# Kernel optimization log

Measured on AMD Instinct MI355X. Metric: run time of the kernel, lower is better.

## Reference

```python
import jax, jax.numpy as jnp
import numpy as np

B, L, H, NH, NE, M = 4, 1024, 768, 12, 42, 8
EMB = 768
OFFSET = 1  # bert cls offset


def setup_inputs() -> dict:
    key = jax.random.key(0)
    ks = jax.random.split(key, 6)
    seq = jax.random.normal(ks[0], (B, L, H), jnp.float32)
    attn = jax.random.uniform(ks[1], (B, NH, L, L), jnp.float32)
    attn = attn / attn.sum(-1, keepdims=True)  # row-stochastic like softmaxed attention probs
    W_head = jax.random.normal(ks[2], (2 * H, EMB), jnp.float32) * 0.02
    b_head = jnp.zeros((EMB,), jnp.float32)
    W_tail = jax.random.normal(ks[3], (2 * H, EMB), jnp.float32) * 0.02
    b_tail = jnp.zeros((EMB,), jnp.float32)
    # mention start positions (before +offset); keep start+offset < L
    mention_pos = jax.random.randint(ks[4], (B, NE, M), 0, L - OFFSET - 1)
    counts = jax.random.randint(ks[5], (B, NE), 1, M + 1)  # >=1 valid mention per entity
    mention_mask = jnp.arange(M)[None, None, :] < counts[:, :, None]
    return dict(sequence_output=seq, attention=attn, W_head=W_head, b_head=b_head,
                W_tail=W_tail, b_tail=b_tail, mention_pos=mention_pos,
                mention_mask=mention_mask)


def _get_hrt(seq, attn, mention_pos, mention_mask):
    # seq: [B,L,H]; attn: [B,NH,L,L]; mention_pos/mask: [B,NE,M]
    b_idx = jnp.arange(B)[:, None, None]
    pos = mention_pos + OFFSET                          # [B,NE,M]
    m_emb = seq[b_idx, pos]                             # [B,NE,M,H] mention embeddings
    att_t = jnp.transpose(attn, (0, 2, 1, 3))           # [B,L,NH,L]
    m_att = att_t[b_idx, pos]                           # [B,NE,M,NH,L] mention attentions
    mask = mention_mask
    neg_inf = jnp.finfo(seq.dtype).min
    # per-entity logsumexp pooling over mentions
    ent_emb = jax.nn.logsumexp(jnp.where(mask[..., None], m_emb, neg_inf), axis=2)
    has_m = mask.any(axis=2)
    ent_emb = jnp.where(has_m[..., None], ent_emb, 0.0)  # [B,NE,H]
    cnt = mask.sum(axis=2).astype(seq.dtype)
    ent_att = (m_att * mask[..., None, None].astype(seq.dtype)).sum(axis=2)
    ent_att = ent_att / jnp.maximum(cnt, 1.0)[..., None, None]  # [B,NE,NH,L] mean over mentions
    # all ordered (head, tail) pairs on the NE x NE grid
    hs = jnp.broadcast_to(ent_emb[:, :, None, :], (B, NE, NE, H))
    ts = jnp.broadcast_to(ent_emb[:, None, :, :], (B, NE, NE, H))
    # ht_att = relu(mean_h(h_att * t_att)), normalized over seq, then context = ht_att @ seq
    ht = jnp.einsum('bihl,bjhl->bijl', ent_att, ent_att) / NH  # [B,NE,NE,L]
    ht = jax.nn.relu(ht)
    ht = ht / (ht.sum(-1, keepdims=True) + 1e-10)
    rs = jnp.einsum('bijl,bld->bijd', ht, seq)                  # [B,NE,NE,H]
    return hs, rs, ts


def reference(sequence_output, attention, W_head, b_head, W_tail, b_tail, mention_pos, mention_mask):
    hs, rs, ts = _get_hrt(sequence_output, attention, mention_pos, mention_mask)
    h_out = jnp.tanh(jnp.concatenate([hs, rs], axis=-1) @ W_head + b_head)
    t_out = jnp.tanh(jnp.concatenate([ts, rs], axis=-1) @ W_tail + b_tail)
    return h_out, t_out
```

## Files before the change

### kernel.cpp

```cpp
#include <hip/hip_runtime.h>
#include <math.h>

typedef _Float16 f16;
typedef __attribute__((ext_vector_type(4))) _Float16 f16x4;
typedef __attribute__((ext_vector_type(8))) _Float16 f16x8;
typedef __attribute__((ext_vector_type(4))) float f32x4;

#define B_    4
#define L_    1024
#define H_    768
#define NH_   12
#define NE_   42
#define M_    8
#define E2_   1536
#define HTP_  1792
#define OUT_HALF 5419008LL

typedef __attribute__((address_space(1))) const unsigned char ga_t;
typedef __attribute__((address_space(3))) unsigned char la_t;
__device__ __forceinline__ void async16(const void* g, void* l) {
    __builtin_amdgcn_global_load_lds((ga_t*)g, (la_t*)l, 16, 0, 0);
}

__device__ __forceinline__ float fast_tanh(float x) {
    float e = __expf(2.f * x);
    return 1.f - 2.f / (e + 1.f);
}


__device__ void prep_body(int bid, char* smem,
                          const float* __restrict__ Wh, const float* __restrict__ Wt,
                          const float* __restrict__ bh, const float* __restrict__ bt,
                          f16* __restrict__ wtop, f16* __restrict__ wbot,
                          float* __restrict__ bcat) {
    float (*tile)[33] = (float(*)[33])smem;
    int tx = bid % 24, ty = (bid / 24) % 24, m = bid / 576;
    const float* src = (m & 1) ? Wt : Wh;
    int roff = (m & 2) ? H_ : 0;
    f16* dst = (m & 2) ? wbot : wtop;
    int coff = (m & 1) ? H_ : 0;
    int x = threadIdx.x & 31, y8 = threadIdx.x >> 5;
#pragma unroll
    for (int r = 0; r < 4; r++) {
        int h = ty*32 + y8 + r*8, c = tx*32 + x;
        tile[y8 + r*8][x] = src[(long long)(roff + h)*H_ + c];
    }
    __syncthreads();
#pragma unroll
    for (int r = 0; r < 4; r++) {
        int c2 = tx*32 + y8 + r*8, h2 = ty*32 + x;
        dst[(long long)(coff + c2)*H_ + h2] = (f16)tile[x][y8 + r*8];
    }
    if (bid == 0) {
        for (int idx = threadIdx.x; idx < E2_; idx += 256)
            bcat[idx] = (idx < H_) ? bh[idx] : bt[idx - H_];
    }
}

__device__ void seq16_body(int bid, const float* __restrict__ seq,
                           f16* __restrict__ seq16) {
    int idx = (bid*256 + threadIdx.x) * 4;
    f32x4 v = *(const f32x4*)(seq + idx);
    f16x4 o = {(f16)v[0], (f16)v[1], (f16)v[2], (f16)v[3]};
    *(f16x4*)(seq16 + idx) = o;
}

__device__ void ent_emb_body(int bid, const float* __restrict__ seq,
                             const int* __restrict__ mpos,
                             const int* __restrict__ mmask,
                             f16* __restrict__ ent) {
    int e = bid % NE_, b = bid / NE_;
    int tid = threadIdx.x;
    const int* mp = mpos  + (b*NE_ + e)*M_;
    const int* mk = mmask + (b*NE_ + e)*M_;
    int pos[M_], msk[M_];
#pragma unroll
    for (int m = 0; m < M_; m++) { msk[m] = mk[m]; pos[m] = mp[m] + 1; }
#pragma unroll
    for (int q = 0; q < 3; q++) {
        int h = tid + q*256;
        float mx = -1e30f, vals[M_];
#pragma unroll
        for (int m = 0; m < M_; m++) {
            vals[m] = 0.f;
            if (msk[m]) {
                float v = seq[((long long)b*L_ + pos[m])*H_ + h];
                vals[m] = v; mx = fmaxf(mx, v);
            }
        }
        float s = 0.f;
#pragma unroll
        for (int m = 0; m < M_; m++) if (msk[m]) s += __expf(vals[m] - mx);
        float lse = (mx > -1e29f) ? mx + __logf(s) : 0.f;
        ent[(b*NE_ + e)*H_ + h] = (f16)lse;
    }
}

__device__ void ent_att_body(int bid, const float* __restrict__ attn,
                             const int* __restrict__ mpos,
                             const int* __restrict__ mmask,
                             f16* __restrict__ eatt) {
    int nh = bid % NH_, e = (bid / NH_) % NE_, b = bid / (NH_*NE_);
    int tid = threadIdx.x;
    int l0 = tid * 4;
    const int* mp = mpos  + (b*NE_ + e)*M_;
    const int* mk = mmask + (b*NE_ + e)*M_;
    const float* abase = attn + (long long)(b*NH_ + nh) * L_ * L_;
    f32x4 acc = {0,0,0,0}; int cnt = 0;
#pragma unroll
    for (int m = 0; m < M_; m++) {
        if (mk[m]) {
            cnt++;
            const float* row = abase + (long long)(mp[m] + 1) * L_;
            acc += *(const f32x4*)(row + l0);
        }
    }
    float inv = 1.f / (float)(cnt > 0 ? cnt : 1);
    f16x4 o = {(f16)(acc[0]*inv), (f16)(acc[1]*inv), (f16)(acc[2]*inv), (f16)(acc[3]*inv)};
    *(f16x4*)(eatt + ((long long)(b*NE_ + e)*NH_ + nh)*L_ + l0) = o;
}

__device__ void ht_body(int bid, char* smem, const f16* __restrict__ eatt,
                        f16* __restrict__ HT) {
    int jg = bid % 6, i = (bid / 6) % NE_, b = bid / 252;
    int tid = threadIdx.x;
    f16* ei_s = (f16*)smem;
    float (*red)[4] = (float(*)[4])(smem + NH_*L_*2);
    const f16* ei = eatt + (long long)(b*NE_ + i)*NH_*L_;
#pragma unroll
    for (int q = 0; q < 6; q++) {
        int off = (q*256 + tid)*8;
        *(f16x8*)(ei_s + off) = *(const f16x8*)(ei + off);
    }
    __syncthreads();
    int l0 = tid*4;
    int wave = tid >> 6, lane = tid & 63;
    for (int jj = 0; jj < 7; jj++) {
        int j = jg*7 + jj;
        const f16* ej = eatt + (long long)(b*NE_ + j)*NH_*L_;
        f32x4 acc = {0,0,0,0};
#pragma unroll
        for (int h = 0; h < NH_; h++) {
            f16x4 vi = *(const f16x4*)(ei_s + h*L_ + l0);
            f16x4 vj = *(const f16x4*)(ej   + h*L_ + l0);
#pragma unroll
            for (int r = 0; r < 4; r++) acc[r] += (float)vi[r] * (float)vj[r];
        }
        float v[4]; float s = 0.f;
#pragma unroll
        for (int r = 0; r < 4; r++) {
            float t = acc[r] * (1.f/12.f);
            t = t > 0.f ? t : 0.f;
            v[r] = t; s += t;
        }
#pragma unroll
        for (int m = 1; m < 64; m <<= 1) s += __shfl_xor(s, m, 64);
        if (lane == 0) red[jj][wave] = s;
        __syncthreads();
        float S = red[jj][0] + red[jj][1] + red[jj][2] + red[jj][3];
        float sc = 1.f / (S + 1e-10f);
        f16x4 o = {(f16)(v[0]*sc), (f16)(v[1]*sc), (f16)(v[2]*sc), (f16)(v[3]*sc)};
        *(f16x4*)(HT + ((long long)b*HTP_ + i*NE_ + j)*L_ + l0) = o;
    }
}

#define LDSS 40
__device__ void gemm_het_body(int bx, int by, char* smem,
                              const f16* __restrict__ A, const f16* __restrict__ BT,
                              float* __restrict__ het, const float* __restrict__ bcat) {
    const int M = 168, K = 768;
    f16* As = (f16*)smem;
    f16* Bs = (f16*)(smem + 64*LDSS*2);
    int bm = bx*64, bn = by*64;
    int tid = threadIdx.x;
    int wave = tid >> 6, lane = tid & 63;
    int wm = (wave >> 1)*32, wn = (wave & 1)*32;
    int lo4 = lane & 15, kq = (lane >> 4)*8;
    int srow = tid >> 2, scol = (tid & 3)*8;
    bool aval = (bm + srow) < M;
    const f16* aptr = A + (long long)(bm + srow)*K + scol;
    const f16* bptr = BT + (long long)(bn + srow)*K + scol;
    f32x4 acc[2][2] = {};
    for (int k0 = 0; k0 < K; k0 += 32) {
        uint4 zero = {0,0,0,0};
        uint4 av = aval ? *(const uint4*)(aptr + k0) : zero;
        uint4 bv = *(const uint4*)(bptr + k0);
        __syncthreads();
        *(uint4*)(As + srow*LDSS + scol) = av;
        *(uint4*)(Bs + srow*LDSS + scol) = bv;
        __syncthreads();
        f16x8 a0 = *(const f16x8*)(As + (wm +      lo4)*LDSS + kq);
        f16x8 a1 = *(const f16x8*)(As + (wm + 16 + lo4)*LDSS + kq);
        f16x8 b0 = *(const f16x8*)(Bs + (wn +      lo4)*LDSS + kq);
        f16x8 b1 = *(const f16x8*)(Bs + (wn + 16 + lo4)*LDSS + kq);
        acc[0][0] = __builtin_amdgcn_mfma_f32_16x16x32_f16(a0, b0, acc[0][0], 0,0,0);
        acc[0][1] = __builtin_amdgcn_mfma_f32_16x16x32_f16(a0, b1, acc[0][1], 0,0,0);
        acc[1][0] = __builtin_amdgcn_mfma_f32_16x16x32_f16(a1, b0, acc[1][0], 0,0,0);
        acc[1][1] = __builtin_amdgcn_mfma_f32_16x16x32_f16(a1, b1, acc[1][1], 0,0,0);
    }
    int rloc = (lane >> 4)*4;
#pragma unroll
    for (int sm = 0; sm < 2; sm++)
#pragma unroll
    for (int sn = 0; sn < 2; sn++) {
        f32x4 a = acc[sm][sn];
        int c  = bn + wn + sn*16 + lo4;
        int rb = bm + wm + sm*16 + rloc;
#pragma unroll
        for (int r = 0; r < 4; r++)
            if (rb + r < M) het[(rb + r)*E2_ + c] = a[r] + bcat[c];
    }
}

template<int MODE>
__device__ void gemm2_body(int bx, int by, int bz, char* smem,
                           const f16* __restrict__ A, const f16* __restrict__ BT, int K,
                           long long strideA, long long strideBT,
                           const float* __restrict__ het, float* __restrict__ outp,
                           f16* __restrict__ outp16) {
    f16* As = (f16*)smem;
    f16* Bs = (f16*)(smem + 8192);
    int bm = bx*128, bn = by*128;
    const f16* Ab = A + strideA*bz;
    const f16* Bb = BT + strideBT*bz;
    int tid = threadIdx.x, wave = tid >> 6, lane = tid & 63;
    int wm = (wave >> 1)*64, wn = (wave & 1)*64;
    int lo4 = lane & 15, kq = (lane >> 4)*8;
    int lrow = lane >> 2, lcol = (lane & 3)*8;
    const f16* ag = Ab + (long long)(bm + wave*32 + lrow)*K + lcol;
    const f16* bg = Bb + (long long)(bn + wave*32 + lrow)*K + lcol;
    f16* asl = As + wave*1024;
    f16* bsl = Bs + wave*1024;
    f32x4 acc[4][4] = {};
    for (int k0 = 0; k0 < K; k0 += 32) {
        async16(ag + k0,          asl);
        async16(ag + k0 + 16*K,   asl + 512);
        async16(bg + k0,          bsl);
        async16(bg + k0 + 16*K,   bsl + 512);
        __syncthreads();
        f16x8 af[4], bf[4];
#pragma unroll
        for (int s = 0; s < 4; s++) {
            af[s] = *(const f16x8*)(As + (wm + s*16 + lo4)*32 + kq);
            bf[s] = *(const f16x8*)(Bs + (wn + s*16 + lo4)*32 + kq);
        }
#pragma unroll
        for (int sm = 0; sm < 4; sm++)
#pragma unroll
        for (int sn = 0; sn < 4; sn++)
            acc[sm][sn] = __builtin_amdgcn_mfma_f32_16x16x32_f16(af[sm], bf[sn], acc[sm][sn], 0,0,0);
        __syncthreads();
    }
    int rloc = (lane >> 4)*4;
#pragma unroll
    for (int sm = 0; sm < 4; sm++)
#pragma unroll
    for (int sn = 0; sn < 4; sn++) {
        f32x4 a = acc[sm][sn];
        int c  = bn + wn + sn*16 + lo4;
        int rb = bm + wm + sm*16 + rloc;
        if constexpr (MODE == 1) {
            f16x4 o = {(f16)a[0], (f16)a[1], (f16)a[2], (f16)a[3]};
            *(f16x4*)(outp16 + (long long)bz*E2_*L_ + (long long)c*L_ + rb) = o;
        } else {
#pragma unroll
            for (int r = 0; r < 4; r++) {
                int row = rb + r;
                if (row < NE_*NE_) {
                    int i = row / NE_;
                    int j = row - i*NE_;
                    int sel = (c < H_) ? i : j;
                    float bias = het[(bz*NE_ + sel)*E2_ + c];
                    float v = fast_tanh(a[r] + bias);
                    long long o = (c < H_)
                        ? ((long long)((bz*NE_ + i)*NE_ + j))*H_ + c
                        : OUT_HALF + ((long long)((bz*NE_ + i)*NE_ + j))*H_ + (c - H_);
                    outp[o] = v;
                }
            }
        }
    }
}

__global__ __launch_bounds__(256) void k_L1(
        const float* __restrict__ seq, const float* __restrict__ attn,
        const float* __restrict__ Wh, const float* __restrict__ bh,
        const float* __restrict__ Wt, const float* __restrict__ bt,
        const int* __restrict__ mpos, const int* __restrict__ mmask,
        f16* __restrict__ wtop, f16* __restrict__ wbot, float* __restrict__ bcat,
        f16* __restrict__ seq16, f16* __restrict__ ent, f16* __restrict__ eatt) {
    __shared__ __align__(16) char smem[4224];
    int bid = blockIdx.x;
    if (bid < 2304)       prep_body(bid, smem, Wh, Wt, bh, bt, wtop, wbot, bcat);
    else if (bid < 5376)  seq16_body(bid - 2304, seq, seq16);
    else if (bid < 5544)  ent_emb_body(bid - 5376, seq, mpos, mmask, ent);
    else                  ent_att_body(bid - 5544, attn, mpos, mmask, eatt);
}

__global__ __launch_bounds__(256) void k_L2(
        const f16* __restrict__ seq16, const f16* __restrict__ wbot,
        const f16* __restrict__ ent, const f16* __restrict__ wtop,
        const float* __restrict__ bcat, const f16* __restrict__ eatt,
        f16* __restrict__ seqWT, float* __restrict__ het, f16* __restrict__ HT) {
    __shared__ __align__(16) char smem[24704];
    int bid = blockIdx.x;
    if (bid < 384) {
        int bx = bid & 7, by = (bid >> 3) % 12, bz = bid / 96;
        gemm2_body<1>(bx, by, bz, smem, seq16, wbot, 768,
                      (long long)L_*H_, 0, nullptr, nullptr, seqWT);
    } else if (bid < 1392) {
        ht_body(bid - 384, smem, eatt, HT);
    } else {
        int r = bid - 1392;
        gemm_het_body(r % 3, r / 3, smem, ent, wtop, het, bcat);
    }
}

__global__ __launch_bounds__(256) void k_L3(
        const f16* __restrict__ HT, const f16* __restrict__ seqWT,
        const float* __restrict__ het, float* __restrict__ outp) {
    __shared__ __align__(16) char smem[16384];
    gemm2_body<2>(blockIdx.x, blockIdx.y, blockIdx.z, smem, HT, seqWT, 1024,
                  (long long)HTP_*L_, (long long)E2_*L_, het, outp, nullptr);
}

extern "C" void kernel_launch(void* const* d_in, const int* in_sizes, int n_in,
                              void* d_out, int out_size, void* d_ws, size_t ws_size,
                              hipStream_t stream) {
    const float* seq  = (const float*)d_in[0];
    const float* attn = (const float*)d_in[1];
    const float* Wh   = (const float*)d_in[2];
    const float* bh   = (const float*)d_in[3];
    const float* Wt   = (const float*)d_in[4];
    const float* bt   = (const float*)d_in[5];
    const int* mpos   = (const int*)d_in[6];
    const int* mmask  = (const int*)d_in[7];
    float* out = (float*)d_out;
    char* ws = (char*)d_ws;
    f16*   ent   = (f16*)  (ws + 0);
    f16*   wtop  = (f16*)  (ws + 258048);
    f16*   wbot  = (f16*)  (ws + 2617344);
    float* bcat  = (float*)(ws + 4976640);
    float* het   = (float*)(ws + 4982784);
    f16*   eatt  = (f16*)  (ws + 6014976);
    f16*   seq16 = (f16*)  (ws + 10143744);
    f16*   HT    = (f16*)  (ws + 16435200);
    f16*   seqWT = (f16*)  (ws + 31115264);

    k_L1<<<7560, 256, 0, stream>>>(seq, attn, Wh, bh, Wt, bt, mpos, mmask,
                                   wtop, wbot, bcat, seq16, ent, eatt);
    k_L2<<<1464, 256, 0, stream>>>(seq16, wbot, ent, wtop, bcat, eatt,
                                   seqWT, het, HT);
    k_L3<<<dim3(14, 12, B_), 256, 0, stream>>>(HT, seqWT, het, out);
}
```

Baseline: 360.4 us.

## Rewrite final GEMM as 256x256 tile, 8-wave kernel with async LDS double buffering

The final HT×seqWT GEMM with tanh epilogue becomes a dedicated kernel. It uses 256x256 tiles, 512 threads, and 128KB of LDS. Global-to-LDS async loads are double-buffered and interleaved per quadrant phase, with explicit vmcnt waits, barriers and setprio around the MFMA bursts, and the LDS layout is XOR-swizzled. The aim is to raise data reuse and overlap memory with MFMA. The cost is fewer blocks (168) on a large-CU GPU, heavy register and LDS pressure, and more fragile manual synchronisation.

New measurement: 371.4 us. 3.1% more time.

```diff
diff --git a/kernel.cpp b/kernel.cpp
--- a/kernel.cpp
+++ b/kernel.cpp
@@ -262,21 +262,140 @@
         if constexpr (MODE == 1) {
             f16x4 o = {(f16)a[0], (f16)a[1], (f16)a[2], (f16)a[3]};
             *(f16x4*)(outp16 + (long long)bz*E2_*L_ + (long long)c*L_ + rb) = o;
-        } else {
-#pragma unroll
-            for (int r = 0; r < 4; r++) {
-                int row = rb + r;
-                if (row < NE_*NE_) {
-                    int i = row / NE_;
-                    int j = row - i*NE_;
-                    int sel = (c < H_) ? i : j;
-                    float bias = het[(bz*NE_ + sel)*E2_ + c];
-                    float v = fast_tanh(a[r] + bias);
-                    long long o = (c < H_)
-                        ? ((long long)((bz*NE_ + i)*NE_ + j))*H_ + c
-                        : OUT_HALF + ((long long)((bz*NE_ + i)*NE_ + j))*H_ + (c - H_);
-                    outp[o] = v;
-                }
+        }
+    }
+}
+
+
+__device__ __forceinline__ void stage_regionA(const f16* __restrict__ Ab, int bm,
+                                              int t, int rq, char* ldsAbuf, int tid) {
+    int k0 = t * 64;
+    char* wbase = ldsAbuf + rq*16384 + (tid & ~63)*16;
+#pragma unroll
+    for (int ld = 0; ld < 2; ld++) {
+        int o    = (ld*512 + tid) * 16;
+        int lr   = o >> 7;
+        int colb = o & 127;
+        int grow = (lr & 63) + ((lr >> 6) << 7) + rq*64;
+        int scolb = colb ^ ((lr & 7) << 4);
+        const char* g = (const char*)(Ab + (long long)(bm + grow)*1024 + k0) + scolb;
+        async16(g, wbase + ld*8192);
+    }
+}
+
+__device__ __forceinline__ void stage_regionB(const f16* __restrict__ Bb, int bn,
+                                              int t, int cq, char* ldsBbuf, int tid) {
+    int k0 = t * 64;
+    char* wbase = ldsBbuf + cq*16384 + (tid & ~63)*16;
+#pragma unroll
+    for (int ld = 0; ld < 2; ld++) {
+        int o    = (ld*512 + tid) * 16;
+        int lr   = o >> 7;
+        int colb = o & 127;
+        int brow = ((lr >> 5)*2 + cq)*32 + (lr & 31);
+        int scolb = colb ^ ((lr & 7) << 4);
+        const char* g = (const char*)(Bb + (long long)(bn + brow)*1024 + k0) + scolb;
+        async16(g, wbase + ld*8192);
+    }
+}
+
+#define PHASE(RQ, CQ, STAGE_STMT, WAIT_STMT) do {                              \
+    f16x8 afr[4][2], bfr[2][2];                                                \
+    _Pragma("unroll")                                                          \
+    for (int i_ = 0; i_ < 4; i_++) {                                           \
+        char* pa_ = bA + (RQ)*16384 + (wr*64 + i_*16 + lo4)*128;               \
+        _Pragma("unroll")                                                      \
+        for (int ks_ = 0; ks_ < 2; ks_++)                                      \
+            afr[i_][ks_] = *(const f16x8*)(pa_ + ((ks_*64 + kq2) ^ sw));       \
+    }                                                                          \
+    _Pragma("unroll")                                                          \
+    for (int j_ = 0; j_ < 2; j_++) {                                           \
+        char* pb_ = bB + (CQ)*16384 + (wc*32 + j_*16 + lo4)*128;               \
+        _Pragma("unroll")                                                      \
+        for (int ks_ = 0; ks_ < 2; ks_++)                                      \
+            bfr[j_][ks_] = *(const f16x8*)(pb_ + ((ks_*64 + kq2) ^ sw));       \
+    }                                                                          \
+    STAGE_STMT;                                                                \
+    __builtin_amdgcn_s_barrier();                                              \
+    __builtin_amdgcn_sched_barrier(0);                                         \
+    asm volatile("" ::: "memory");                                             \
+    __builtin_amdgcn_s_setprio(1);                                             \
+    _Pragma("unroll")                                                          \
+    for (int i_ = 0; i_ < 4; i_++)                                             \
+    _Pragma("unroll")                                                          \
+    for (int j_ = 0; j_ < 2; j_++) {                                           \
+        acc[(RQ)*4+i_][(CQ)*2+j_] = __builtin_amdgcn_mfma_f32_16x16x32_f16(    \
+            afr[i_][0], bfr[j_][0], acc[(RQ)*4+i_][(CQ)*2+j_], 0,0,0);         \
+        acc[(RQ)*4+i_][(CQ)*2+j_] = __builtin_amdgcn_mfma_f32_16x16x32_f16(    \
+            afr[i_][1], bfr[j_][1], acc[(RQ)*4+i_][(CQ)*2+j_], 0,0,0);         \
+    }                                                                          \
+    __builtin_amdgcn_s_setprio(0);                                             \
+    WAIT_STMT;                                                                 \
+    __builtin_amdgcn_s_barrier();                                              \
+    __builtin_amdgcn_sched_barrier(0);                                         \
+    asm volatile("" ::: "memory");                                             \
+} while (0)
+
+__global__ __launch_bounds__(512, 2) void k_L3(
+        const f16* __restrict__ HT, const f16* __restrict__ seqWT,
+        const float* __restrict__ het, float* __restrict__ outp) {
+    __shared__ __align__(16) char smem[131072];
+    int bm = blockIdx.x*256, bn = blockIdx.y*256, bz = blockIdx.z;
+    const f16* Ab = HT + (long long)HTP_*L_*bz;
+    const f16* Bb = seqWT + (long long)E2_*L_*bz;
+    int tid = threadIdx.x, wave = tid >> 6, lane = tid & 63;
+    int wr = wave >> 2, wc = wave & 3;
+    int lo4 = lane & 15, kq2 = (lane >> 4)*16;
+    int sw = (lo4 & 7) << 4;
+    f32x4 acc[8][4] = {};
+
+    stage_regionA(Ab, bm, 0, 0, smem + 0,     tid);
+    stage_regionB(Bb, bn, 0, 0, smem + 65536, tid);
+    stage_regionB(Bb, bn, 0, 1, smem + 65536, tid);
+    stage_regionA(Ab, bm, 0, 1, smem + 0,     tid);
+    stage_regionA(Ab, bm, 1, 0, smem + 32768, tid);
+    asm volatile("s_waitcnt vmcnt(2)" ::: "memory");
+    __builtin_amdgcn_s_barrier();
+    __builtin_amdgcn_sched_barrier(0);
+    asm volatile("" ::: "memory");
+
+    for (int t = 0; t < 16; t++) {
+        char* bA  = smem + (t & 1)*32768;
+        char* bB  = smem + 65536 + (t & 1)*32768;
+        char* bA1 = smem + ((t+1) & 1)*32768;
+        char* bB1 = smem + 65536 + ((t+1) & 1)*32768;
+        bool s1 = (t+1 < 16), s2 = (t+2 < 16);
+
+        PHASE(0, 0, { if (s1) stage_regionB(Bb, bn, t+1, 0, bB1, tid); }, {});
+        PHASE(0, 1, { if (s1) stage_regionB(Bb, bn, t+1, 1, bB1, tid); },
+              { if (t < 15) { asm volatile("s_waitcnt vmcnt(4)" ::: "memory"); }
+                else        { asm volatile("s_waitcnt vmcnt(0)" ::: "memory"); } });
+        PHASE(1, 0, { if (s2) stage_regionA(Ab, bm, t+2, 0, bA, tid); }, {});
+        PHASE(1, 1, { if (s1) stage_regionA(Ab, bm, t+1, 1, bA1, tid); },
+              { if (t < 15) { asm volatile("s_waitcnt vmcnt(4)" ::: "memory"); } });
+    }
+
+    int rloc = (lane >> 4)*4;
+#pragma unroll
+    for (int sm = 0; sm < 8; sm++)
+#pragma unroll
+    for (int sn = 0; sn < 4; sn++) {
+        f32x4 a = acc[sm][sn];
+        int c  = bn + wc*64 + sn*16 + lo4;
+        int rb = bm + wr*128 + sm*16 + rloc;
+#pragma unroll
+        for (int r = 0; r < 4; r++) {
+            int row = rb + r;
+            if (row < NE_*NE_) {
+                int i = row / NE_;
+                int j = row - i*NE_;
+                int sel = (c < H_) ? i : j;
+                float bias = het[(bz*NE_ + sel)*E2_ + c];
+                float v = fast_tanh(a[r] + bias);
+                long long o = (c < H_)
+                    ? ((long long)((bz*NE_ + i)*NE_ + j))*H_ + c
+                    : OUT_HALF + ((long long)((bz*NE_ + i)*NE_ + j))*H_ + (c - H_);
+                outp[o] = v;
             }
         }
     }
@@ -314,14 +433,6 @@
         int r = bid - 1392;
         gemm_het_body(r % 3, r / 3, smem, ent, wtop, het, bcat);
     }
-}
-
-__global__ __launch_bounds__(256) void k_L3(
-        const f16* __restrict__ HT, const f16* __restrict__ seqWT,
-        const float* __restrict__ het, float* __restrict__ outp) {
-    __shared__ __align__(16) char smem[16384];
-    gemm2_body<2>(blockIdx.x, blockIdx.y, blockIdx.z, smem, HT, seqWT, 1024,
-                  (long long)HTP_*L_, (long long)E2_*L_, het, outp, nullptr);
 }
 
 extern "C" void kernel_launch(void* const* d_in, const int* in_sizes, int n_in,
@@ -351,5 +462,5 @@
                                    wtop, wbot, bcat, seq16, ent, eatt);
     k_L2<<<1464, 256, 0, stream>>>(seq16, wbot, ent, wtop, bcat, eatt,
                                    seqWT, het, HT);
-    k_L3<<<dim3(14, 12, B_), 256, 0, stream>>>(HT, seqWT, het, out);
-}
+    k_L3<<<dim3(7, 6, B_), 512, 0, stream>>>(HT, seqWT, het, out);
+}
```
